# Kernel tuning notes

Hardware: AMD Instinct MI355X
Metric: run time of the kernel (lower is better)

Reference implementation:

```python
import jax, jax.numpy as jnp
import numpy as np

N = 2000      # batch_size * num_rois
PS = 7        # pool_size
C = 256       # roi-align channels
HID = 1024    # head width
NC = 81       # num_classes (COCO incl. background)
EPS = 1e-3    # keras BatchNormalization default epsilon


def setup_inputs() -> dict:
    key = jax.random.key(0)
    ks = jax.random.split(key, 6)
    sc = lambda k, shape, s: jax.random.normal(k, shape, jnp.float32) * s
    return {
        "pooled_rois": jax.random.normal(ks[0], (N, PS, PS, C), jnp.float32),
        # 7x7 VALID conv on a 7x7 input == flattened dense: [PS*PS*C, HID]
        "w1": sc(ks[1], (PS * PS * C, HID), 0.01),
        "b1": jnp.zeros((HID,), jnp.float32),
        "gamma1": jnp.ones((HID,), jnp.float32),
        "beta1": jnp.zeros((HID,), jnp.float32),
        # 1x1 conv == dense [HID, HID]
        "w2": sc(ks[2], (HID, HID), 0.02),
        "b2": jnp.zeros((HID,), jnp.float32),
        "gamma2": jnp.ones((HID,), jnp.float32),
        "beta2": jnp.zeros((HID,), jnp.float32),
        "w_logits": sc(ks[3], (HID, NC), 0.02),
        "b_logits": jnp.zeros((NC,), jnp.float32),
        "w_delta": sc(ks[4], (HID, NC * 4), 0.02),
        "b_delta": jnp.zeros((NC * 4,), jnp.float32),
    }


def _batchnorm_train(x, gamma, beta):
    # training=True: normalize with batch statistics over the RoI axis
    mu = jnp.mean(x, axis=0)
    var = jnp.var(x, axis=0)
    return gamma * (x - mu) * jax.lax.rsqrt(var + EPS) + beta


def reference(pooled_rois, w1, b1, gamma1, beta1, w2, b2, gamma2, beta2,
              w_logits, b_logits, w_delta, b_delta):
    n = pooled_rois.shape[0]
    # rcnn_class_conv1: 7x7 VALID conv on 7x7 input -> flatten + matmul
    x = pooled_rois.reshape(n, -1) @ w1 + b1          # [N, 1024]
    x = jax.nn.relu(_batchnorm_train(x, gamma1, beta1))
    # rcnn_class_conv2: 1x1 conv -> matmul
    x = x @ w2 + b2                                    # [N, 1024]
    x = jax.nn.relu(_batchnorm_train(x, gamma2, beta2))
    logits = x @ w_logits + b_logits                   # [N, NC]
    probs = jax.nn.softmax(logits, axis=-1)            # [N, NC]
    deltas = (x @ w_delta + b_delta).reshape(n, NC, 4) # [N, NC, 4]
    return logits, probs, deltas
```

## Files before the change

kernel.cpp:

```cpp
#include <hip/hip_runtime.h>

typedef unsigned short u16;
typedef __bf16 bf16x8 __attribute__((ext_vector_type(8)));
typedef float f32x4 __attribute__((ext_vector_type(4)));
typedef u16 u16x8 __attribute__((ext_vector_type(8)));

static constexpr int kNRoi = 2000;
static constexpr int kMPad = 2048;
static constexpr int kKin  = 12544;
static constexpr int kHid  = 1024;
static constexpr int kNOutPad = 512;
static constexpr int kNC = 81;
static constexpr int kND = 324;


__device__ __forceinline__ u16 f2bf(float f) {
  union { float f; unsigned u; } v; v.f = f;
  unsigned r = v.u + 0x7fffu + ((v.u >> 16) & 1u);
  return (u16)(r >> 16);
}

__device__ __forceinline__ void transpose64(const float* __restrict__ in,
                                            u16* __restrict__ out, int R, int C,
                                            int bx, int by, u16* t, int tid) {
  const int cb = bx * 64, rb = by * 64;
  const int rl = tid >> 4, cl = (tid & 15) * 4;
#pragma unroll
  for (int i = 0; i < 4; ++i) {
    int r = rl + i * 16;
    f32x4 v = *(const f32x4*)(in + (long)(rb + r) * C + cb + cl);
#pragma unroll
    for (int j = 0; j < 4; ++j) t[(cl + j) * 72 + r] = f2bf(v[j]);
  }
  __syncthreads();
  const int c2 = tid >> 3, r2 = (tid & 7) * 8;
#pragma unroll
  for (int i = 0; i < 2; ++i) {
    int c = c2 + i * 32;
    u16x8 v = *(const u16x8*)&t[c * 72 + r2];
    *(u16x8*)(out + (long)(cb + c) * R + rb + r2) = v;
  }
}

__device__ __forceinline__ void transpose32(const float* __restrict__ in,
                                            u16* __restrict__ out, int R, int C,
                                            int bx, int by, u16* t, int tid) {
  int tx = tid & 31, ty = tid >> 5;
  int cb = bx * 32, rb = by * 32;
#pragma unroll
  for (int i = 0; i < 4; ++i) {
    int r = rb + ty + i * 8, c = cb + tx;
    if (r < R && c < C) t[(ty + i * 8) * 33 + tx] = f2bf(in[(long)r * C + c]);
  }
  __syncthreads();
#pragma unroll
  for (int i = 0; i < 4; ++i) {
    int c = cb + ty + i * 8, r = rb + tx;
    if (c < C && r < R) out[(long)c * R + r] = t[tx * 33 + ty + i * 8];
  }
}

__global__ __launch_bounds__(256) void prep(
    const float* __restrict__ pooled, const float* __restrict__ w1,
    const float* __restrict__ w2, const float* __restrict__ wl,
    const float* __restrict__ wd, u16* __restrict__ A1,
    u16* __restrict__ W1T, u16* __restrict__ W2T, u16* __restrict__ WHT,
    float* __restrict__ X1, float* __restrict__ S) {
  __shared__ u16 sh[64 * 72];
  const int tid = threadIdx.x;
  int id = blockIdx.x;
  if (id < 12250) {
    long i = ((long)id * 256 + tid) * 8;
    f32x4 a = *(const f32x4*)(pooled + i);
    f32x4 b = *(const f32x4*)(pooled + i + 4);
    u16x8 h;
#pragma unroll
    for (int j = 0; j < 4; ++j) { h[j] = f2bf(a[j]); h[4 + j] = f2bf(b[j]); }
    *(u16x8*)(A1 + i) = h;
    return;
  }
  id -= 12250;
  if (id < 3136) { transpose64(w1, W1T, kKin, kHid, id & 15, id >> 4, sh, tid); return; }
  id -= 3136;
  if (id < 256)  { transpose64(w2, W2T, kHid, kHid, id & 15, id >> 4, sh, tid); return; }
  id -= 256;
  if (id < 96)   { transpose32(wl, WHT, kHid, kNC, id % 3, id / 3, sh, tid); return; }
  id -= 96;
  if (id < 352)  { transpose32(wd, WHT + kNC * kHid, kHid, kND, id % 11, id / 11, sh, tid); return; }
  id -= 352;
  if (id < 54) {
    int idx = id * 256 + tid;
    if (idx < 13696) *(u16x8*)(WHT + 405 * kHid + idx * 8) = (u16x8){};
    return;
  }
  id -= 54;
  if (id < 2048) {
    *(f32x4*)(X1 + ((long)id * 256 + tid) * 4) = (f32x4){};
    return;
  }
  id -= 2048;
  *(f32x4*)(S + ((long)id * 256 + tid) * 4) = (f32x4){};
}

__global__ __launch_bounds__(256) void gemm_bt(
    const u16* __restrict__ A, const u16* __restrict__ Bt,
    float* __restrict__ C, int Mreal, int K, int N, int kchunk) {
  __shared__ u16 As[2][128 * 32];
  __shared__ u16 Bs[2][128 * 32];
  const int tid  = threadIdx.x;
  const int lane = tid & 63;
  const int wave = tid >> 6;
  const int wm = (wave >> 1) * 64;
  const int wn = (wave & 1) * 64;

  f32x4 acc[4][4] = {};

  const int r0 = tid >> 2;
  const int kc = (tid & 3) * 8;
  long ar0 = (long)blockIdx.x * 128 + r0;      if (ar0 > Mreal - 1) ar0 = Mreal - 1;
  long ar1 = (long)blockIdx.x * 128 + 64 + r0; if (ar1 > Mreal - 1) ar1 = Mreal - 1;
  const long br0 = (long)blockIdx.y * 128 + r0;
  const long br1 = br0 + 64;

  const int kb = blockIdx.z * kchunk;
  const u16* ag0 = A + ar0 * K + kb + kc;
  const u16* ag1 = A + ar1 * K + kb + kc;
  const u16* bg0 = Bt + br0 * K + kb + kc;
  const u16* bg1 = Bt + br1 * K + kb + kc;

  const int fr = lane & 15;
  const int fq = (lane >> 4) * 8;
  const int iters = kchunk / 32;

#define STAGE(b) do {                                                          \
    u16* al_ = As[b] + wave * 512;                                             \
    u16* bl_ = Bs[b] + wave * 512;                                             \
    __builtin_amdgcn_global_load_lds((const __attribute__((address_space(1))) void*)ag0, \
                                     (__attribute__((address_space(3))) void*)al_, 16, 0, 0); \
    __builtin_amdgcn_global_load_lds((const __attribute__((address_space(1))) void*)ag1, \
                                     (__attribute__((address_space(3))) void*)(al_ + 2048), 16, 0, 0); \
    __builtin_amdgcn_global_load_lds((const __attribute__((address_space(1))) void*)bg0, \
                                     (__attribute__((address_space(3))) void*)bl_, 16, 0, 0); \
    __builtin_amdgcn_global_load_lds((const __attribute__((address_space(1))) void*)bg1, \
                                     (__attribute__((address_space(3))) void*)(bl_ + 2048), 16, 0, 0); \
    ag0 += 32; ag1 += 32; bg0 += 32; bg1 += 32;                                \
  } while (0)

  STAGE(0);
  int buf = 0;
  for (int it = 0; it < iters; ++it) {
    __syncthreads();
    if (it + 1 < iters) STAGE(buf ^ 1);

    const u16* as_ = As[buf];
    const u16* bs_ = Bs[buf];
    bf16x8 afr[4], bfr[4];
#pragma unroll
    for (int i = 0; i < 4; ++i)
      afr[i] = *(const bf16x8*)(as_ + (wm + i * 16 + fr) * 32 + fq);
#pragma unroll
    for (int i = 0; i < 4; ++i)
      bfr[i] = *(const bf16x8*)(bs_ + (wn + i * 16 + fr) * 32 + fq);
#pragma unroll
    for (int mi = 0; mi < 4; ++mi)
#pragma unroll
      for (int ni = 0; ni < 4; ++ni)
        acc[mi][ni] = __builtin_amdgcn_mfma_f32_16x16x32_bf16(afr[mi], bfr[ni], acc[mi][ni], 0, 0, 0);
    buf ^= 1;
  }
#undef STAGE

  const int row0 = blockIdx.x * 128 + wm + (lane >> 4) * 4;
  const int col0 = blockIdx.y * 128 + wn + fr;
#pragma unroll
  for (int mi = 0; mi < 4; ++mi)
#pragma unroll
    for (int ni = 0; ni < 4; ++ni)
#pragma unroll
      for (int e = 0; e < 4; ++e)
        atomicAdd(&C[(long)(row0 + mi * 16 + e) * N + col0 + ni * 16], acc[mi][ni][e]);
}

__global__ __launch_bounds__(256) void colstats_zero(
    const float* __restrict__ X, float* __restrict__ S, float* __restrict__ SS,
    float* __restrict__ Z) {
  int id = blockIdx.x;
  if (id < 320) {
    int c = (id & 3) * 256 + threadIdx.x;
    int r0 = (id >> 2) * 25;
    float s = 0.f, ss = 0.f;
    for (int r = r0; r < r0 + 25; ++r) {
      float v = X[(long)r * kHid + c];
      s += v; ss += v * v;
    }
    atomicAdd(&S[c], s);
    atomicAdd(&SS[c], ss);
  } else {
    id -= 320;
    *(f32x4*)(Z + ((long)id * 256 + threadIdx.x) * 4) = (f32x4){};
  }
}

__global__ __launch_bounds__(256) void bn_relu(
    const float* __restrict__ X, const float* __restrict__ S,
    const float* __restrict__ SS, const float* __restrict__ gamma,
    const float* __restrict__ beta, u16* __restrict__ H) {
  constexpr float invN = 1.f / (float)kNRoi;
  long i = ((long)blockIdx.x * 256 + threadIdx.x) * 8;
  int c = (int)(i & (kHid - 1));
  f32x4 x0 = *(const f32x4*)(X + i);
  f32x4 x1 = *(const f32x4*)(X + i + 4);
  f32x4 s0 = *(const f32x4*)(S + c),    s1 = *(const f32x4*)(S + c + 4);
  f32x4 q0 = *(const f32x4*)(SS + c),   q1 = *(const f32x4*)(SS + c + 4);
  f32x4 g0 = *(const f32x4*)(gamma + c), g1 = *(const f32x4*)(gamma + c + 4);
  f32x4 b0 = *(const f32x4*)(beta + c),  b1 = *(const f32x4*)(beta + c + 4);
  u16x8 h;
#pragma unroll
  for (int j = 0; j < 4; ++j) {
    float mu = s0[j] * invN;
    float var = q0[j] * invN - mu * mu;
    float sc = g0[j] * rsqrtf(var + 1e-3f);
    h[j] = f2bf(fmaxf(0.f, sc * x0[j] + (b0[j] - mu * sc)));
    mu = s1[j] * invN;
    var = q1[j] * invN - mu * mu;
    sc = g1[j] * rsqrtf(var + 1e-3f);
    h[4 + j] = f2bf(fmaxf(0.f, sc * x1[j] + (b1[j] - mu * sc)));
  }
  *(u16x8*)(H + i) = h;
}

__global__ __launch_bounds__(256) void head_out(
    const float* __restrict__ X, const float* __restrict__ bl,
    const float* __restrict__ bd, float* __restrict__ out) {
  int lane = threadIdx.x & 63;
  int row = blockIdx.x * 4 + (threadIdx.x >> 6);
  if (row >= kNRoi) return;
  const float* xr = X + (long)row * kNOutPad;
  float v0 = xr[lane] + bl[lane];
  float v1 = (lane < kNC - 64) ? xr[64 + lane] + bl[64 + lane] : -3.0e38f;
  float m = fmaxf(v0, v1);
#pragma unroll
  for (int off = 32; off > 0; off >>= 1) m = fmaxf(m, __shfl_xor(m, off, 64));
  float e0 = __expf(v0 - m);
  float e1 = (lane < kNC - 64) ? __expf(v1 - m) : 0.f;
  float s = e0 + e1;
#pragma unroll
  for (int off = 32; off > 0; off >>= 1) s += __shfl_xor(s, off, 64);
  float inv = 1.f / s;
  float* lo = out + (long)row * kNC;
  float* pr = out + (long)kNRoi * kNC + (long)row * kNC;
  float* de = out + 2L * kNRoi * kNC + (long)row * kND;
  lo[lane] = v0;
  pr[lane] = e0 * inv;
  if (lane < kNC - 64) { lo[64 + lane] = v1; pr[64 + lane] = e1 * inv; }
#pragma unroll
  for (int j = 0; j < 5; ++j) {
    int c = lane + 64 * j;
    de[c] = xr[kNC + c] + bd[c];
  }
  if (lane < 4) { int c = lane + 320; de[c] = xr[kNC + c] + bd[c]; }
}

extern "C" void kernel_launch(void* const* d_in, const int* in_sizes, int n_in,
                              void* d_out, int out_size, void* d_ws, size_t ws_size,
                              hipStream_t stream) {
  const float* pooled   = (const float*)d_in[0];
  const float* w1       = (const float*)d_in[1];
  const float* gamma1   = (const float*)d_in[3];
  const float* beta1    = (const float*)d_in[4];
  const float* w2       = (const float*)d_in[5];
  const float* gamma2   = (const float*)d_in[7];
  const float* beta2    = (const float*)d_in[8];
  const float* w_logits = (const float*)d_in[9];
  const float* b_logits = (const float*)d_in[10];
  const float* w_delta  = (const float*)d_in[11];
  const float* b_delta  = (const float*)d_in[12];

  char* ws = (char*)d_ws;
  u16*   W1T  = (u16*)(ws + 0);
  u16*   W2T  = (u16*)(ws + 25690112);
  u16*   WHT  = (u16*)(ws + 27787264);
  float* X1   = (float*)(ws + 28835840);
  u16*   H    = (u16*)(ws + 37224448);
  float* S    = (float*)(ws + 41418752);
  u16*   A1   = (u16*)(ws + 41435136);
  float* X2   = (float*)(ws + 41435136);
  float* XOUT = (float*)(ws + 49823744);

  float* S1  = S;
  float* SS1 = S + 1024;
  float* S2  = S + 2048;
  float* SS2 = S + 3072;

  prep<<<18196, 256, 0, stream>>>(pooled, w1, w2, w_logits, w_delta,
                                  A1, W1T, W2T, WHT, X1, S);

  gemm_bt<<<dim3(16, 8, 8), 256, 0, stream>>>(A1, W1T, X1, kNRoi, kKin, kHid, kKin / 8);

  colstats_zero<<<320 + 3072, 256, 0, stream>>>(X1, S1, SS1, X2);
  bn_relu<<<(kMPad * kHid) / 2048, 256, 0, stream>>>(X1, S1, SS1, gamma1, beta1, H);

  gemm_bt<<<dim3(16, 8, 4), 256, 0, stream>>>(H, W2T, X2, kMPad, kHid, kHid, kHid / 4);

  colstats_zero<<<320, 256, 0, stream>>>(X2, S2, SS2, nullptr);
  bn_relu<<<(kMPad * kHid) / 2048, 256, 0, stream>>>(X2, S2, SS2, gamma2, beta2, H);

  gemm_bt<<<dim3(16, 4, 4), 256, 0, stream>>>(H, WHT, XOUT, kMPad, kHid, kNOutPad, kHid / 4);

  head_out<<<kNRoi / 4, 256, 0, stream>>>(XOUT, b_logits, b_delta, (float*)d_out);
}
```

Measured before the change: 390.3 us.

## Swizzle LDS tile layout and remap GEMM block order for XCD locality

The GEMM kernel now XOR-swizzles the k-chunk position within each 32-element LDS row, both when staging global loads and when reading MFMA fragments. This is meant to cut LDS bank conflicts on the fragment reads. The grid is also flattened to 1D, with a custom mapping that places adjacent M tiles and the same N/K tiles on the same XCD (block id mod 8), aiming for better L2 reuse of A and B. The risk is that the remapping shifts scheduling balance, and the swizzle has to match the global_load_lds destination layout exactly.

```diff
diff --git a/kernel.cpp b/kernel.cpp
--- a/kernel.cpp
+++ b/kernel.cpp
@@ -104,7 +104,8 @@
 
 __global__ __launch_bounds__(256) void gemm_bt(
     const u16* __restrict__ A, const u16* __restrict__ Bt,
-    float* __restrict__ C, int Mreal, int K, int N, int kchunk) {
+    float* __restrict__ C, int Mreal, int K, int N, int kchunk,
+    int gy, int gz) {
   __shared__ u16 As[2][128 * 32];
   __shared__ u16 Bs[2][128 * 32];
   const int tid  = threadIdx.x;
@@ -113,16 +114,24 @@
   const int wm = (wave >> 1) * 64;
   const int wn = (wave & 1) * 64;
 
+  const int bl = blockIdx.x;
+  const int k8 = bl & 7;
+  const int sq = bl >> 3;
+  const int by = sq % gy;
+  const int tq = sq / gy;
+  const int bx = 2 * k8 + (tq & 1);
+  const int bz = tq >> 1;
+
   f32x4 acc[4][4] = {};
 
   const int r0 = tid >> 2;
-  const int kc = (tid & 3) * 8;
-  long ar0 = (long)blockIdx.x * 128 + r0;      if (ar0 > Mreal - 1) ar0 = Mreal - 1;
-  long ar1 = (long)blockIdx.x * 128 + 64 + r0; if (ar1 > Mreal - 1) ar1 = Mreal - 1;
-  const long br0 = (long)blockIdx.y * 128 + r0;
+  const int kc = ((tid & 3) ^ ((r0 >> 1) & 3)) * 8;
+  long ar0 = (long)bx * 128 + r0;      if (ar0 > Mreal - 1) ar0 = Mreal - 1;
+  long ar1 = (long)bx * 128 + 64 + r0; if (ar1 > Mreal - 1) ar1 = Mreal - 1;
+  const long br0 = (long)by * 128 + r0;
   const long br1 = br0 + 64;
 
-  const int kb = blockIdx.z * kchunk;
+  const int kb = bz * kchunk;
   const u16* ag0 = A + ar0 * K + kb + kc;
   const u16* ag1 = A + ar1 * K + kb + kc;
   const u16* bg0 = Bt + br0 * K + kb + kc;
@@ -130,6 +139,7 @@
 
   const int fr = lane & 15;
   const int fq = (lane >> 4) * 8;
+  const int fqs = fq ^ (((fr >> 1) & 3) << 3);
   const int iters = kchunk / 32;
 
 #define STAGE(b) do {                                                          \
@@ -157,10 +167,10 @@
     bf16x8 afr[4], bfr[4];
 #pragma unroll
     for (int i = 0; i < 4; ++i)
-      afr[i] = *(const bf16x8*)(as_ + (wm + i * 16 + fr) * 32 + fq);
+      afr[i] = *(const bf16x8*)(as_ + (wm + i * 16 + fr) * 32 + fqs);
 #pragma unroll
     for (int i = 0; i < 4; ++i)
-      bfr[i] = *(const bf16x8*)(bs_ + (wn + i * 16 + fr) * 32 + fq);
+      bfr[i] = *(const bf16x8*)(bs_ + (wn + i * 16 + fr) * 32 + fqs);
 #pragma unroll
     for (int mi = 0; mi < 4; ++mi)
 #pragma unroll
@@ -170,8 +180,8 @@
   }
 #undef STAGE
 
-  const int row0 = blockIdx.x * 128 + wm + (lane >> 4) * 4;
-  const int col0 = blockIdx.y * 128 + wn + fr;
+  const int row0 = bx * 128 + wm + (lane >> 4) * 4;
+  const int col0 = by * 128 + wn + fr;
 #pragma unroll
   for (int mi = 0; mi < 4; ++mi)
 #pragma unroll
@@ -295,17 +305,17 @@
   prep<<<18196, 256, 0, stream>>>(pooled, w1, w2, w_logits, w_delta,
                                   A1, W1T, W2T, WHT, X1, S);
 
-  gemm_bt<<<dim3(16, 8, 8), 256, 0, stream>>>(A1, W1T, X1, kNRoi, kKin, kHid, kKin / 8);
+  gemm_bt<<<1024, 256, 0, stream>>>(A1, W1T, X1, kNRoi, kKin, kHid, kKin / 8, 8, 8);
 
   colstats_zero<<<320 + 3072, 256, 0, stream>>>(X1, S1, SS1, X2);
   bn_relu<<<(kMPad * kHid) / 2048, 256, 0, stream>>>(X1, S1, SS1, gamma1, beta1, H);
 
-  gemm_bt<<<dim3(16, 8, 4), 256, 0, stream>>>(H, W2T, X2, kMPad, kHid, kHid, kHid / 4);
+  gemm_bt<<<512, 256, 0, stream>>>(H, W2T, X2, kMPad, kHid, kHid, kHid / 4, 8, 4);
 
   colstats_zero<<<320, 256, 0, stream>>>(X2, S2, SS2, nullptr);
   bn_relu<<<(kMPad * kHid) / 2048, 256, 0, stream>>>(X2, S2, SS2, gamma2, beta2, H);
 
-  gemm_bt<<<dim3(16, 4, 4), 256, 0, stream>>>(H, WHT, XOUT, kMPad, kHid, kNOutPad, kHid / 4);
+  gemm_bt<<<256, 256, 0, stream>>>(H, WHT, XOUT, kMPad, kHid, kNOutPad, kHid / 4, 4, 4);
 
   head_out<<<kNRoi / 4, 256, 0, stream>>>(XOUT, b_logits, b_delta, (float*)d_out);
 }
```

Result: no change. 388.5 us (-0.5%).

## Replace 128x128 split-K GEMM with 256x256-tile swizzled-LDS GEMM

Applied to the files above, without the earlier changes.

Replaces the GEMM kernel with one using 256x256 output tiles, 512 threads, BK=64, XOR-swizzled LDS layout and a 1D grid with uneven split-K distribution over K tiles. The inner loop interleaves fragment loads with MFMA quadrants under sched_barrier and setprio, with explicit vmcnt waits and barriers. The larger tile raises data reuse per LDS load and reduces global traffic. In exchange it uses 64 KB of LDS and more accumulator registers per thread, which can limit occupancy, and yields fewer blocks for the smaller GEMMs.

```diff
diff --git a/kernel.cpp b/kernel.cpp
--- a/kernel.cpp
+++ b/kernel.cpp
@@ -102,83 +102,131 @@
   *(f32x4*)(S + ((long)id * 256 + tid) * 4) = (f32x4){};
 }
 
-__global__ __launch_bounds__(256) void gemm_bt(
+__global__ __launch_bounds__(512, 2) void gemm256(
     const u16* __restrict__ A, const u16* __restrict__ Bt,
-    float* __restrict__ C, int Mreal, int K, int N, int kchunk) {
-  __shared__ u16 As[2][128 * 32];
-  __shared__ u16 Bs[2][128 * 32];
+    float* __restrict__ C, int Mreal, int K, int N,
+    int gy, int ntPer, int ntRem) {
+  __shared__ u16 As[2][16384];
+  __shared__ u16 Bs[2][16384];
+
   const int tid  = threadIdx.x;
   const int lane = tid & 63;
-  const int wave = tid >> 6;
-  const int wm = (wave >> 1) * 64;
-  const int wn = (wave & 1) * 64;
-
-  f32x4 acc[4][4] = {};
-
-  const int r0 = tid >> 2;
-  const int kc = (tid & 3) * 8;
-  long ar0 = (long)blockIdx.x * 128 + r0;      if (ar0 > Mreal - 1) ar0 = Mreal - 1;
-  long ar1 = (long)blockIdx.x * 128 + 64 + r0; if (ar1 > Mreal - 1) ar1 = Mreal - 1;
-  const long br0 = (long)blockIdx.y * 128 + r0;
-  const long br1 = br0 + 64;
-
-  const int kb = blockIdx.z * kchunk;
-  const u16* ag0 = A + ar0 * K + kb + kc;
-  const u16* ag1 = A + ar1 * K + kb + kc;
-  const u16* bg0 = Bt + br0 * K + kb + kc;
-  const u16* bg1 = Bt + br1 * K + kb + kc;
-
-  const int fr = lane & 15;
-  const int fq = (lane >> 4) * 8;
-  const int iters = kchunk / 32;
+  const int w    = tid >> 6;
+  const int wm   = (w >> 2) * 128;
+  const int wn   = (w & 3) * 64;
+
+  const int bl = blockIdx.x;
+  const int bx = bl & 7;
+  const int sq = bl >> 3;
+  const int by = sq % gy;
+  const int z  = sq / gy;
+  const int ktBase = z * ntPer + (z < ntRem ? z : ntRem);
+  const int NT = ntPer + (z < ntRem ? 1 : 0);
+  const long kb = (long)ktBase * 64;
+
+  const int rA  = w * 8 + (lane >> 3);
+  const int cgs = (lane & 7) ^ (rA & 7);
+  const u16* ap[4];
+  const u16* bp[4];
+#pragma unroll
+  for (int j = 0; j < 4; ++j) {
+    int rloc = rA + j * 64;
+    long arow = (long)bx * 256 + rloc; if (arow > Mreal - 1) arow = Mreal - 1;
+    ap[j] = A + arow * K + kb + cgs * 8;
+    long brow = (long)by * 256 + rloc;
+    bp[j] = Bt + brow * K + kb + cgs * 8;
+  }
 
 #define STAGE(b) do {                                                          \
-    u16* al_ = As[b] + wave * 512;                                             \
-    u16* bl_ = Bs[b] + wave * 512;                                             \
-    __builtin_amdgcn_global_load_lds((const __attribute__((address_space(1))) void*)ag0, \
-                                     (__attribute__((address_space(3))) void*)al_, 16, 0, 0); \
-    __builtin_amdgcn_global_load_lds((const __attribute__((address_space(1))) void*)ag1, \
-                                     (__attribute__((address_space(3))) void*)(al_ + 2048), 16, 0, 0); \
-    __builtin_amdgcn_global_load_lds((const __attribute__((address_space(1))) void*)bg0, \
-                                     (__attribute__((address_space(3))) void*)bl_, 16, 0, 0); \
-    __builtin_amdgcn_global_load_lds((const __attribute__((address_space(1))) void*)bg1, \
-                                     (__attribute__((address_space(3))) void*)(bl_ + 2048), 16, 0, 0); \
-    ag0 += 32; ag1 += 32; bg0 += 32; bg1 += 32;                                \
+    _Pragma("unroll") for (int j_ = 0; j_ < 4; ++j_) {                         \
+      __builtin_amdgcn_global_load_lds(                                        \
+          (const __attribute__((address_space(1))) void*)ap[j_],               \
+          (__attribute__((address_space(3))) void*)(&As[b][w * 512 + j_ * 4096]), 16, 0, 0); \
+      __builtin_amdgcn_global_load_lds(                                        \
+          (const __attribute__((address_space(1))) void*)bp[j_],               \
+          (__attribute__((address_space(3))) void*)(&Bs[b][w * 512 + j_ * 4096]), 16, 0, 0); \
+      ap[j_] += 64; bp[j_] += 64;                                              \
+    }                                                                          \
   } while (0)
 
+  const int fr   = lane & 15;
+  const int q    = lane >> 4;
+  const int swzr = fr & 7;
+
+  f32x4 acc[8][4] = {};
+
+#define LDA(mg) do { _Pragma("unroll")                                         \
+    for (int i_ = 0; i_ < 4; ++i_) {                                           \
+      const u16* p_ = as_ + (wm + (mg) * 64 + i_ * 16 + fr) * 64;              \
+      af[i_][0] = *(const bf16x8*)(p_ + ((q ^ swzr) * 8));                     \
+      af[i_][1] = *(const bf16x8*)(p_ + (((4 + q) ^ swzr) * 8));               \
+    } } while (0)
+
+#define LDB(dst, ng) do { _Pragma("unroll")                                    \
+    for (int i_ = 0; i_ < 2; ++i_) {                                           \
+      const u16* p_ = bs_ + (wn + (ng) * 32 + i_ * 16 + fr) * 64;              \
+      dst[i_][0] = *(const bf16x8*)(p_ + ((q ^ swzr) * 8));                    \
+      dst[i_][1] = *(const bf16x8*)(p_ + (((4 + q) ^ swzr) * 8));              \
+    } } while (0)
+
+#define QUAD(mg, ng, B_) do {                                                  \
+    __builtin_amdgcn_s_setprio(1);                                             \
+    _Pragma("unroll") for (int mi_ = 0; mi_ < 4; ++mi_)                        \
+    _Pragma("unroll") for (int ni_ = 0; ni_ < 2; ++ni_)                        \
+    _Pragma("unroll") for (int kk_ = 0; kk_ < 2; ++kk_)                        \
+      acc[(mg) * 4 + mi_][(ng) * 2 + ni_] =                                    \
+          __builtin_amdgcn_mfma_f32_16x16x32_bf16(                             \
+              af[mi_][kk_], B_[ni_][kk_],                                      \
+              acc[(mg) * 4 + mi_][(ng) * 2 + ni_], 0, 0, 0);                   \
+    __builtin_amdgcn_s_setprio(0);                                             \
+  } while (0)
+
   STAGE(0);
+  asm volatile("s_waitcnt vmcnt(0)" ::: "memory");
+  __builtin_amdgcn_s_barrier();
+  __builtin_amdgcn_sched_barrier(0);
+
   int buf = 0;
-  for (int it = 0; it < iters; ++it) {
-    __syncthreads();
-    if (it + 1 < iters) STAGE(buf ^ 1);
+  for (int t = 0; t < NT; ++t) {
+    if (t + 1 < NT) STAGE(buf ^ 1);
 
     const u16* as_ = As[buf];
     const u16* bs_ = Bs[buf];
-    bf16x8 afr[4], bfr[4];
-#pragma unroll
-    for (int i = 0; i < 4; ++i)
-      afr[i] = *(const bf16x8*)(as_ + (wm + i * 16 + fr) * 32 + fq);
-#pragma unroll
-    for (int i = 0; i < 4; ++i)
-      bfr[i] = *(const bf16x8*)(bs_ + (wn + i * 16 + fr) * 32 + fq);
-#pragma unroll
-    for (int mi = 0; mi < 4; ++mi)
-#pragma unroll
-      for (int ni = 0; ni < 4; ++ni)
-        acc[mi][ni] = __builtin_amdgcn_mfma_f32_16x16x32_bf16(afr[mi], bfr[ni], acc[mi][ni], 0, 0, 0);
+    bf16x8 af[4][2], bn0[2][2], bn1[2][2];
+
+    LDA(0); LDB(bn0, 0);
+    QUAD(0, 0, bn0);
+    __builtin_amdgcn_sched_barrier(0);
+    LDB(bn1, 1);
+    QUAD(0, 1, bn1);
+    __builtin_amdgcn_sched_barrier(0);
+    LDA(1);
+    QUAD(1, 1, bn1);
+    __builtin_amdgcn_sched_barrier(0);
+    QUAD(1, 0, bn0);
+
+    if (t + 1 < NT) {
+      asm volatile("s_waitcnt vmcnt(0)" ::: "memory");
+      __builtin_amdgcn_s_barrier();
+      __builtin_amdgcn_sched_barrier(0);
+    }
     buf ^= 1;
   }
 #undef STAGE
-
-  const int row0 = blockIdx.x * 128 + wm + (lane >> 4) * 4;
-  const int col0 = blockIdx.y * 128 + wn + fr;
-#pragma unroll
-  for (int mi = 0; mi < 4; ++mi)
+#undef LDA
+#undef LDB
+#undef QUAD
+
+  const int row0 = bx * 256 + wm + q * 4;
+  const int col0 = by * 256 + wn + fr;
+#pragma unroll
+  for (int mi = 0; mi < 8; ++mi)
 #pragma unroll
     for (int ni = 0; ni < 4; ++ni)
 #pragma unroll
       for (int e = 0; e < 4; ++e)
-        atomicAdd(&C[(long)(row0 + mi * 16 + e) * N + col0 + ni * 16], acc[mi][ni][e]);
+        atomicAdd(&C[(long)(row0 + mi * 16 + e) * N + col0 + ni * 16],
+                  acc[mi][ni][e]);
 }
 
 __global__ __launch_bounds__(256) void colstats_zero(
@@ -295,17 +343,17 @@
   prep<<<18196, 256, 0, stream>>>(pooled, w1, w2, w_logits, w_delta,
                                   A1, W1T, W2T, WHT, X1, S);
 
-  gemm_bt<<<dim3(16, 8, 8), 256, 0, stream>>>(A1, W1T, X1, kNRoi, kKin, kHid, kKin / 8);
+  gemm256<<<256, 512, 0, stream>>>(A1, W1T, X1, kNRoi, kKin, kHid, 4, 24, 4);
 
   colstats_zero<<<320 + 3072, 256, 0, stream>>>(X1, S1, SS1, X2);
   bn_relu<<<(kMPad * kHid) / 2048, 256, 0, stream>>>(X1, S1, SS1, gamma1, beta1, H);
 
-  gemm_bt<<<dim3(16, 8, 4), 256, 0, stream>>>(H, W2T, X2, kMPad, kHid, kHid, kHid / 4);
+  gemm256<<<256, 512, 0, stream>>>(H, W2T, X2, kMPad, kHid, kHid, 4, 2, 0);
 
   colstats_zero<<<320, 256, 0, stream>>>(X2, S2, SS2, nullptr);
   bn_relu<<<(kMPad * kHid) / 2048, 256, 0, stream>>>(X2, S2, SS2, gamma2, beta2, H);
 
-  gemm_bt<<<dim3(16, 4, 4), 256, 0, stream>>>(H, WHT, XOUT, kMPad, kHid, kNOutPad, kHid / 4);
+  gemm256<<<256, 512, 0, stream>>>(H, WHT, XOUT, kMPad, kHid, kNOutPad, 2, 1, 0);
 
   head_out<<<kNRoi / 4, 256, 0, stream>>>(XOUT, b_logits, b_delta, (float*)d_out);
 }
```

Result: slower. 450.7 us (+15.5%).
